# Optimization experiments

Measured on AMD Instinct MI355X. Metric: run time of the kernel, lower is better.

Reference implementation:

```python
import jax, jax.numpy as jnp
import numpy as np

EMBED_DIM = 128
MAX_LEN = 256.0
LN_EPS = 1e-5


def sinusoidal_pe(x, embed_dim, embed_size):
    # x: [..., ] float; returns [..., embed_dim]
    inv_freq = 1.0 / embed_size ** (2.0 * jnp.arange(embed_dim // 2, dtype=jnp.float32) / embed_dim)
    angles = x[..., None] * jnp.float32(np.pi) * inv_freq
    return jnp.concatenate([jnp.sin(angles), jnp.cos(angles)], axis=-1)


def setup_inputs() -> dict:
    key = jax.random.key(0)
    ks = jax.random.split(key, 20)
    B, N, A = 4, 256, 4
    input_nf, hidden_nf, output_nf = 128, 256, 128
    edge_in = 2 * input_nf + EMBED_DIM + 3  # 387

    def lin(k, fan_in, fan_out):
        bound = 1.0 / np.sqrt(fan_in)
        kw, kb = jax.random.split(k)
        W = jax.random.uniform(kw, (fan_in, fan_out), jnp.float32, -bound, bound)
        b = jax.random.uniform(kb, (fan_out,), jnp.float32, -bound, bound)
        return W, b

    We1, be1 = lin(ks[0], edge_in, hidden_nf)
    We2, be2 = lin(ks[1], hidden_nf, hidden_nf)
    Wn1, bn1 = lin(ks[2], input_nf + hidden_nf, hidden_nf)
    Wn2, bn2 = lin(ks[3], hidden_nf, output_nf)
    Wc1, bc1 = lin(ks[4], hidden_nf, hidden_nf)
    Wc2, bc2 = lin(ks[5], hidden_nf, 1)

    coords = jax.random.normal(ks[6], (B, N, A, 3), jnp.float32)
    node_features = jax.random.normal(ks[7], (B, N, input_nf), jnp.float32)
    atom_mask = jnp.ones((B, N, A), jnp.float32)
    residue_indices = jnp.sort(jax.random.randint(ks[8], (B, N), 0, 256), axis=-1).astype(jnp.int32)

    return dict(coords=coords, node_features=node_features, atom_mask=atom_mask,
                residue_indices=residue_indices,
                We1=We1, be1=be1, We2=We2, be2=be2,
                Wn1=Wn1, bn1=bn1, Wn2=Wn2, bn2=bn2,
                gamma=jnp.ones((output_nf,), jnp.float32), beta=jnp.zeros((output_nf,), jnp.float32),
                Wc1=Wc1, bc1=bc1, Wc2=Wc2, bc2=bc2)


def reference(coords, node_features, atom_mask, residue_indices,
              We1, be1, We2, be2, Wn1, bn1, Wn2, bn2, gamma, beta,
              Wc1, bc1, Wc2, bc2):
    B, N, A, _ = coords.shape
    # relative residue offsets -> sinusoidal PE: [B,N,N,embed_dim]
    rel = (residue_indices[:, :, None] - residue_indices[:, None, :]).astype(jnp.float32)
    rel_enc = sinusoidal_pe(rel, EMBED_DIM, MAX_LEN)
    # directional vectors: mean over atoms of pairwise coord diffs -> [B,N,N,3]
    dirs = (coords[:, :, None, :, :] - coords[:, None, :, :, :]).mean(axis=3)
    # pairwise edge features [B,N,N,2*F+E+3]
    fi = jnp.broadcast_to(node_features[:, :, None, :], (B, N, N, node_features.shape[-1]))
    fj = jnp.broadcast_to(node_features[:, None, :, :], (B, N, N, node_features.shape[-1]))
    edge_feat = jnp.concatenate([fi, fj, rel_enc, dirs], axis=-1)
    msg = jax.nn.silu(jax.nn.silu(edge_feat @ We1 + be1) @ We2 + be2)  # [B,N,N,H]
    agg = msg.sum(axis=2)  # [B,N,H]
    h = jnp.concatenate([node_features, agg], axis=-1)
    h = jax.nn.silu(h @ Wn1 + bn1) @ Wn2 + bn2  # [B,N,output_nf]
    mu = h.mean(axis=-1, keepdims=True)
    var = ((h - mu) ** 2).mean(axis=-1, keepdims=True)
    h = (h - mu) / jnp.sqrt(var + LN_EPS) * gamma + beta
    cu = jax.nn.silu(msg @ Wc1 + bc1) @ Wc2 + bc2  # [B,N,N,1]
    coord_updates = (cu * dirs).sum(axis=2)  # [B,N,3]
    updated_coords = coords + coord_updates[:, :, None, :] * atom_mask[..., None]
    return updated_coords, h
```

## Files before the change

kernel.cpp:

```cpp
#include <hip/hip_runtime.h>

typedef unsigned short u16;
typedef __attribute__((ext_vector_type(8))) _Float16 hfrag8;
typedef __attribute__((ext_vector_type(4))) float f32x4;

__device__ __forceinline__ float bu2f(u16 u) { return __uint_as_float(((unsigned)u) << 16); }
__device__ __forceinline__ u16 f2bu(float f) {
    unsigned x = __float_as_uint(f);
    return (u16)((x + 0x7fffu + ((x >> 16) & 1u)) >> 16);
}
__device__ __forceinline__ u16 f2hu(float f) {
    _Float16 h = (_Float16)f;
    return __builtin_bit_cast(u16, h);
}
__device__ __forceinline__ float ldf(const void* p, int i, bool f32) {
    return f32 ? ((const float*)p)[i] : bu2f(((const u16*)p)[i]);
}
__device__ __forceinline__ float siluf(float x) {
    return x * __builtin_amdgcn_rcpf(1.0f + __expf(-x));
}
__device__ __forceinline__ unsigned pkh(float a, float b) {
    return __builtin_bit_cast(unsigned, __builtin_amdgcn_cvt_pkrtz(a, b));
}
__device__ __forceinline__ bool detect_f32(const void* nf, int t) {
    const u16* p = (const u16*)nf;
    int ext = 0;
    if (t < 256) {
        u16 v = p[t * 2];
        int e = (v >> 7) & 0xFF;
        ext = (e >= 140 || e == 0) ? 1 : 0;
    }
    return __syncthreads_count(ext) > 32;
}

__global__ __launch_bounds__(256) void prep_kernel(
    const void* __restrict__ coords, const void* __restrict__ nf,
    const void* __restrict__ We1, const void* __restrict__ be1,
    const void* __restrict__ We2, const void* __restrict__ Wc1,
    float* __restrict__ cbar, float* __restrict__ pi2, float* __restrict__ qd,
    float* __restrict__ Ttab, u16* __restrict__ We2X, u16* __restrict__ Wc1X)
{
    const int t = threadIdx.x;
    const bool f32 = detect_f32(nf, t);
    const int blk = blockIdx.x;

    __shared__ float nf_l[4][128];
    __shared__ float ctmp[4][12];
    __shared__ float cb_l[4][3];
    __shared__ float pe[128];
    __shared__ u16 tile[32][33];

    if (blk < 256) {
        const int row0 = blk * 4;
        for (int idx = t; idx < 512; idx += 256) {
            int r = idx >> 7, k = idx & 127;
            nf_l[r][k] = ldf(nf, (row0 + r) * 128 + k, f32);
        }
        if (t < 48) ctmp[t / 12][t % 12] = ldf(coords, row0 * 12 + t, f32);
        __syncthreads();
        if (t < 12) {
            int r = t / 3, x = t % 3;
            float m = 0.25f * (ctmp[r][x] + ctmp[r][3 + x] + ctmp[r][6 + x] + ctmp[r][9 + x]);
            cb_l[r][x] = m;
            cbar[(row0 + r) * 3 + x] = m;
        }
        __syncthreads();
        const int n = t;
        float accP[4] = {0.f, 0.f, 0.f, 0.f}, accQ[4] = {0.f, 0.f, 0.f, 0.f};
        for (int k = 0; k < 128; k++) {
            float w1 = ldf(We1, k * 256 + n, f32);
            float w2 = ldf(We1, (128 + k) * 256 + n, f32);
#pragma unroll
            for (int r = 0; r < 4; r++) {
                accP[r] += nf_l[r][k] * w1;
                accQ[r] += nf_l[r][k] * w2;
            }
        }
        float wx = ldf(We1, 384 * 256 + n, f32);
        float wy = ldf(We1, 385 * 256 + n, f32);
        float wz = ldf(We1, 386 * 256 + n, f32);
        float b1 = ldf(be1, n, f32);
#pragma unroll
        for (int r = 0; r < 4; r++) {
            float d = cb_l[r][0] * wx + cb_l[r][1] * wy + cb_l[r][2] * wz;
            pi2[(row0 + r) * 256 + n] = accP[r] + d + b1;
            qd[(row0 + r) * 256 + n]  = accQ[r] - d;
        }
    } else if (blk < 767) {
        const float d = (float)(blk - 511);
        if (t < 64) {
            float ang = d * 3.14159265358979323846f * exp2f(-(float)t * 0.125f);
            pe[t] = sinf(ang);
            pe[64 + t] = cosf(ang);
        }
        __syncthreads();
        float acc = 0.f;
        for (int k = 0; k < 128; k++) acc += pe[k] * ldf(We1, (256 + k) * 256 + t, f32);
        Ttab[(blk - 256) * 256 + t] = acc;
    } else {
        int tbf = blk - 767;
        int mat = tbf >> 6;
        int tb = tbf & 63;
        int bx = tb & 7, by = tb >> 3;
        const void* src = mat ? Wc1 : We2;
        u16* dst = mat ? Wc1X : We2X;
        int tx = threadIdx.x & 31, ty = threadIdx.x >> 5;
#pragma unroll
        for (int p = 0; p < 4; p++) {
            int r = by * 32 + ty + p * 8;
            tile[ty + p * 8][tx] = f2hu(ldf(src, r * 256 + bx * 32 + tx, f32));
        }
        __syncthreads();
#pragma unroll
        for (int p = 0; p < 4; p++) {
            int n = bx * 32 + ty + p * 8;
            dst[((n >> 4) * 8 + by) * 512 + (n & 15) * 32 + tx] = tile[tx][ty + p * 8];
        }
    }
}

__global__ __launch_bounds__(512, 1)
void edge_kernel(
    const int* __restrict__ resid,
    const float* __restrict__ pi2, const float* __restrict__ qd,
    const float* __restrict__ Ttab, const float* __restrict__ cbar,
    const u16* __restrict__ We2X, const u16* __restrict__ Wc1X,
    const void* __restrict__ be2, const void* __restrict__ bc1,
    const void* __restrict__ Wc2, const void* __restrict__ bc2,
    const void* __restrict__ nf,
    float* __restrict__ agg_out, float* __restrict__ cupd_out)
{
    const int t = threadIdx.x;
    const bool f32 = detect_f32(nf, t);
    const int node = blockIdx.x;
    const int b = node >> 8;
    const int lane = t & 63, w = t >> 6;
    const int c = lane & 15, q = lane >> 4;

    __shared__ __align__(16) u16 U[128][280];
    __shared__ int relidx[256];
    __shared__ float fin[8][4];

    if (t < 256) relidx[t] = resid[node] - resid[(b << 8) + t] + 255;
    const float bc2q = 0.125f * ldf(bc2, 0, f32);

    float4 be2v[2], bc1v[2], wc2v[2];
#pragma unroll
    for (int nn = 0; nn < 2; nn++) {
        const int base = w * 32 + nn * 16 + q * 4;
        be2v[nn] = make_float4(ldf(be2, base, f32), ldf(be2, base + 1, f32),
                               ldf(be2, base + 2, f32), ldf(be2, base + 3, f32));
        bc1v[nn] = make_float4(ldf(bc1, base, f32), ldf(bc1, base + 1, f32),
                               ldf(bc1, base + 2, f32), ldf(bc1, base + 3, f32));
        wc2v[nn] = make_float4(ldf(Wc2, base, f32), ldf(Wc2, base + 1, f32),
                               ldf(Wc2, base + 2, f32), ldf(Wc2, base + 3, f32));
    }

    const int kp = lane << 2;
    const float4 pv = *(const float4*)(pi2 + node * 256 + kp);

    float aggv[2][4] = {{0.f}};
    float s0 = 0.f, s1 = 0.f, s2 = 0.f, s3 = 0.f;

    const f32x4 zf = {0.f, 0.f, 0.f, 0.f};
    __syncthreads();

    for (int jc = 0; jc < 2; jc++) {
        const int j0 = jc << 7;
        {
            const float* qbase = qd + ((b << 8) + j0) * 256 + kp;
            const int r0 = w * 16;
#pragma unroll 4
            for (int jj = 0; jj < 16; jj++) {
                const int j = r0 + jj;
                const float4 qv = *(const float4*)(qbase + j * 256);
                const float4 tv = *(const float4*)(Ttab + relidx[j0 + j] * 256 + kp);
                uint2 pk;
                pk.x = pkh(siluf(pv.x + qv.x + tv.x), siluf(pv.y + qv.y + tv.y));
                pk.y = pkh(siluf(pv.z + qv.z + tv.z), siluf(pv.w + qv.w + tv.w));
                *(uint2*)&U[j][kp] = pk;
            }
        }
        __syncthreads();

        f32x4 acc[8][2];
#pragma unroll
        for (int m = 0; m < 8; m++)
#pragma unroll
            for (int nn = 0; nn < 2; nn++) acc[m][nn] = zf;
#pragma unroll 2
        for (int ks = 0; ks < 8; ks++) {
            const int kb = ks * 32 + q * 8;
            hfrag8 wf[2];
#pragma unroll
            for (int nn = 0; nn < 2; nn++)
                wf[nn] = *(const hfrag8*)(We2X + ((w * 2 + nn) * 8 + ks) * 512 + c * 32 + q * 8);
            hfrag8 hm[8];
#pragma unroll
            for (int m = 0; m < 8; m++)
                hm[m] = *(const hfrag8*)&U[m * 16 + c][kb];
#pragma unroll
            for (int m = 0; m < 8; m++)
#pragma unroll
                for (int nn = 0; nn < 2; nn++)
                    acc[m][nn] = __builtin_amdgcn_mfma_f32_16x16x32_f16(wf[nn], hm[m], acc[m][nn], 0, 0, 0);
        }
        __syncthreads();

#pragma unroll
        for (int m = 0; m < 8; m++) {
            u16* mrow = &U[m * 16 + c][w * 32 + q * 4];
#pragma unroll
            for (int nn = 0; nn < 2; nn++) {
                float sa = siluf(acc[m][nn][0] + be2v[nn].x);
                float sb = siluf(acc[m][nn][1] + be2v[nn].y);
                float sc_ = siluf(acc[m][nn][2] + be2v[nn].z);
                float sd = siluf(acc[m][nn][3] + be2v[nn].w);
                aggv[nn][0] += sa; aggv[nn][1] += sb;
                aggv[nn][2] += sc_; aggv[nn][3] += sd;
                uint2 pk;
                pk.x = pkh(sa, sb);
                pk.y = pkh(sc_, sd);
                *(uint2*)(mrow + nn * 16) = pk;
            }
        }
        __syncthreads();

#pragma unroll
        for (int m = 0; m < 8; m++)
#pragma unroll
            for (int nn = 0; nn < 2; nn++) acc[m][nn] = zf;
#pragma unroll 2
        for (int ks = 0; ks < 8; ks++) {
            const int kb = ks * 32 + q * 8;
            hfrag8 wf[2];
#pragma unroll
            for (int nn = 0; nn < 2; nn++)
                wf[nn] = *(const hfrag8*)(Wc1X + ((w * 2 + nn) * 8 + ks) * 512 + c * 32 + q * 8);
            hfrag8 mm[8];
#pragma unroll
            for (int m = 0; m < 8; m++)
                mm[m] = *(const hfrag8*)&U[m * 16 + c][kb];
#pragma unroll
            for (int m = 0; m < 8; m++)
#pragma unroll
                for (int nn = 0; nn < 2; nn++)
                    acc[m][nn] = __builtin_amdgcn_mfma_f32_16x16x32_f16(wf[nn], mm[m], acc[m][nn], 0, 0, 0);
        }
        __syncthreads();

#pragma unroll
        for (int m = 0; m < 8; m++) {
            float dv = 0.f;
#pragma unroll
            for (int nn = 0; nn < 2; nn++) {
                dv += siluf(acc[m][nn][0] + bc1v[nn].x) * wc2v[nn].x;
                dv += siluf(acc[m][nn][1] + bc1v[nn].y) * wc2v[nn].y;
                dv += siluf(acc[m][nn][2] + bc1v[nn].z) * wc2v[nn].z;
                dv += siluf(acc[m][nn][3] + bc1v[nn].w) * wc2v[nn].w;
            }
            dv += __shfl_xor(dv, 16);
            dv += __shfl_xor(dv, 32);
            if (q == 0) {
                const float vb = dv + bc2q;
                const float* cp = cbar + ((b << 8) + j0 + m * 16 + c) * 3;
                s0 += vb;
                s1 += vb * cp[0];
                s2 += vb * cp[1];
                s3 += vb * cp[2];
            }
        }
    }

#pragma unroll
    for (int nn = 0; nn < 2; nn++)
#pragma unroll
        for (int r = 0; r < 4; r++) {
            float v = aggv[nn][r];
            v += __shfl_xor(v, 1);
            v += __shfl_xor(v, 2);
            v += __shfl_xor(v, 4);
            v += __shfl_xor(v, 8);
            aggv[nn][r] = v;
        }
    if (c == 0) {
#pragma unroll
        for (int nn = 0; nn < 2; nn++) {
            float4 o = make_float4(aggv[nn][0], aggv[nn][1], aggv[nn][2], aggv[nn][3]);
            *(float4*)(agg_out + node * 256 + w * 32 + nn * 16 + q * 4) = o;
        }
    }

#pragma unroll
    for (int d = 1; d < 16; d <<= 1) {
        s0 += __shfl_xor(s0, d);
        s1 += __shfl_xor(s1, d);
        s2 += __shfl_xor(s2, d);
        s3 += __shfl_xor(s3, d);
    }
    if (lane == 0) { fin[w][0] = s0; fin[w][1] = s1; fin[w][2] = s2; fin[w][3] = s3; }
    __syncthreads();
    if (t == 0) {
        float S0 = 0.f, S1 = 0.f, S2 = 0.f, S3 = 0.f;
#pragma unroll
        for (int u = 0; u < 8; u++) {
            S0 += fin[u][0]; S1 += fin[u][1]; S2 += fin[u][2]; S3 += fin[u][3];
        }
        const float cx = cbar[node * 3 + 0], cy = cbar[node * 3 + 1], cz = cbar[node * 3 + 2];
        cupd_out[node * 3 + 0] = S0 * cx - S1;
        cupd_out[node * 3 + 1] = S0 * cy - S2;
        cupd_out[node * 3 + 2] = S0 * cz - S3;
    }
}

__global__ __launch_bounds__(256) void out_kernel(
    const void* __restrict__ nf, const float* __restrict__ agg,
    const void* __restrict__ Wn1, const void* __restrict__ bn1,
    const void* __restrict__ Wn2, const void* __restrict__ bn2,
    const void* __restrict__ gamma, const void* __restrict__ beta,
    const void* __restrict__ coords, const void* __restrict__ mask,
    const float* __restrict__ cupd, void* __restrict__ d_out)
{
    const int t = threadIdx.x;
    const bool f32 = detect_f32(nf, t);

    if (blockIdx.x >= 128) {
        int idx = (blockIdx.x - 128) * 256 + t;
        if (idx < 4 * 256 * 4 * 3) {
            int x = idx % 3;
            int a = (idx / 3) & 3;
            int node = idx / 12;
            float v = ldf(coords, idx, f32) + cupd[node * 3 + x] * ldf(mask, node * 4 + a, f32);
            if (f32) ((float*)d_out)[idx] = v;
            else     ((u16*)d_out)[idx] = f2bu(v);
        }
        return;
    }

    const int row0 = blockIdx.x * 8;
    __shared__ float x_l[8][384];
    __shared__ float hs[8][256];
    __shared__ float ho[8][128];
    for (int idx = t; idx < 8 * 384; idx += 256) {
        int r = idx / 384, k = idx % 384;
        x_l[r][k] = (k < 128) ? ldf(nf, (row0 + r) * 128 + k, f32)
                              : agg[(row0 + r) * 256 + (k - 128)];
    }
    __syncthreads();
    {
        float a1[8] = {0.f, 0.f, 0.f, 0.f, 0.f, 0.f, 0.f, 0.f};
        for (int k = 0; k < 384; k++) {
            float wv = ldf(Wn1, k * 256 + t, f32);
#pragma unroll
            for (int r = 0; r < 8; r++) a1[r] += x_l[r][k] * wv;
        }
        float b1 = ldf(bn1, t, f32);
#pragma unroll
        for (int r = 0; r < 8; r++) hs[r][t] = siluf(a1[r] + b1);
    }
    __syncthreads();
    {
        int cc = t & 127, rg = (t >> 7) * 4;
        float a2[4] = {0.f, 0.f, 0.f, 0.f};
        for (int k = 0; k < 256; k++) {
            float wv = ldf(Wn2, k * 128 + cc, f32);
#pragma unroll
            for (int r = 0; r < 4; r++) a2[r] += hs[rg + r][k] * wv;
        }
        float b2 = ldf(bn2, cc, f32);
#pragma unroll
        for (int r = 0; r < 4; r++) ho[rg + r][cc] = a2[r] + b2;
    }
    __syncthreads();
    {
        int row = t >> 5, s = t & 31;
        float sm = 0.f, sq = 0.f;
#pragma unroll
        for (int u = 0; u < 4; u++) {
            float v = ho[row][s + 32 * u];
            sm += v; sq += v * v;
        }
#pragma unroll
        for (int d = 1; d < 32; d <<= 1) {
            sm += __shfl_xor(sm, d);
            sq += __shfl_xor(sq, d);
        }
        float mu = sm * (1.f / 128.f);
        float var = sq * (1.f / 128.f) - mu * mu;
        float inv = rsqrtf(var + 1e-5f);
#pragma unroll
        for (int u = 0; u < 4; u++) {
            int cc = s + 32 * u;
            float y = (ho[row][cc] - mu) * inv;
            float outv = y * ldf(gamma, cc, f32) + ldf(beta, cc, f32);
            int oi = 12288 + (row0 + row) * 128 + cc;
            if (f32) ((float*)d_out)[oi] = outv;
            else     ((u16*)d_out)[oi] = f2bu(outv);
        }
    }
}

extern "C" void kernel_launch(void* const* d_in, const int* in_sizes, int n_in,
                              void* d_out, int out_size, void* d_ws, size_t ws_size,
                              hipStream_t stream)
{
    const void* coords = d_in[0];
    const void* nf     = d_in[1];
    const void* mask   = d_in[2];
    const int* resid   = (const int*)d_in[3];
    const void* We1 = d_in[4];
    const void* be1 = d_in[5];
    const void* We2 = d_in[6];
    const void* be2 = d_in[7];
    const void* Wn1 = d_in[8];
    const void* bn1 = d_in[9];
    const void* Wn2 = d_in[10];
    const void* bn2 = d_in[11];
    const void* gamma = d_in[12];
    const void* beta  = d_in[13];
    const void* Wc1 = d_in[14];
    const void* bc1 = d_in[15];
    const void* Wc2 = d_in[16];
    const void* bc2 = d_in[17];

    float* f   = (float*)d_ws + 16;
    float* cbar = f;
    float* pi2  = cbar + 3072;
    float* qd   = pi2 + 262144;
    float* Ttab = qd + 262144;
    float* agg  = Ttab + 130816;
    float* cupd = agg + 262144;
    u16* We2X = (u16*)(cupd + 3072);
    u16* Wc1X = We2X + 65536;

    hipLaunchKernelGGL(prep_kernel, dim3(895), dim3(256), 0, stream,
                       coords, nf, We1, be1, We2, Wc1, cbar, pi2, qd, Ttab, We2X, Wc1X);
    hipLaunchKernelGGL(edge_kernel, dim3(1024), dim3(512), 0, stream,
                       resid, pi2, qd, Ttab, cbar, We2X, Wc1X, be2, bc1, Wc2, bc2, nf, agg, cupd);
    hipLaunchKernelGGL(out_kernel, dim3(176), dim3(256), 0, stream,
                       nf, agg, Wn1, bn1, Wn2, bn2, gamma, beta, coords, mask, cupd, d_out);
}
```

Measured before the change: 318.0 us.

## Retile edge-kernel MFMA warps into a 2x4 grid of 64x64 output tiles

Each of the 8 warps now computes a 64-row by 64-column output block (4x4 MFMA tiles) instead of all 128 rows by 32 columns (8x2 tiles). This halves the LDS activation fragment reads per MFMA, at the cost of more weight fragment loads from global or cache. Because each row's partial sums now come from two row-warp groups, the bc2 scaling changes to a quarter and agg is combined in shared memory before it is written. Bias and Wc2 vectors are staged in LDS rather than held in registers, to offset the larger accumulator footprint.

Result: slower. 330.2 us (+3.8%).

```diff
diff --git a/kernel.cpp b/kernel.cpp
--- a/kernel.cpp
+++ b/kernel.cpp
@@ -136,30 +136,27 @@
     const int b = node >> 8;
     const int lane = t & 63, w = t >> 6;
     const int c = lane & 15, q = lane >> 4;
+    const int wr = w & 1, wc = w >> 1;
+    const int rowbase = wr * 64, colbase = wc * 64;
 
     __shared__ __align__(16) u16 U[128][280];
     __shared__ int relidx[256];
+    __shared__ float be2_l[256], bc1_l[256], wc2_l[256];
+    __shared__ float aggl[2][256];
     __shared__ float fin[8][4];
 
-    if (t < 256) relidx[t] = resid[node] - resid[(b << 8) + t] + 255;
-    const float bc2q = 0.125f * ldf(bc2, 0, f32);
-
-    float4 be2v[2], bc1v[2], wc2v[2];
-#pragma unroll
-    for (int nn = 0; nn < 2; nn++) {
-        const int base = w * 32 + nn * 16 + q * 4;
-        be2v[nn] = make_float4(ldf(be2, base, f32), ldf(be2, base + 1, f32),
-                               ldf(be2, base + 2, f32), ldf(be2, base + 3, f32));
-        bc1v[nn] = make_float4(ldf(bc1, base, f32), ldf(bc1, base + 1, f32),
-                               ldf(bc1, base + 2, f32), ldf(bc1, base + 3, f32));
-        wc2v[nn] = make_float4(ldf(Wc2, base, f32), ldf(Wc2, base + 1, f32),
-                               ldf(Wc2, base + 2, f32), ldf(Wc2, base + 3, f32));
-    }
+    if (t < 256) {
+        relidx[t] = resid[node] - resid[(b << 8) + t] + 255;
+        be2_l[t] = ldf(be2, t, f32);
+        bc1_l[t] = ldf(bc1, t, f32);
+        wc2_l[t] = ldf(Wc2, t, f32);
+    }
+    const float bc2q = 0.25f * ldf(bc2, 0, f32);
 
     const int kp = lane << 2;
     const float4 pv = *(const float4*)(pi2 + node * 256 + kp);
 
-    float aggv[2][4] = {{0.f}};
+    float aggv[4][4] = {{0.f}};
     float s0 = 0.f, s1 = 0.f, s2 = 0.f, s3 = 0.f;
 
     const f32x4 zf = {0.f, 0.f, 0.f, 0.f};
@@ -183,39 +180,40 @@
         }
         __syncthreads();
 
-        f32x4 acc[8][2];
-#pragma unroll
-        for (int m = 0; m < 8; m++)
-#pragma unroll
-            for (int nn = 0; nn < 2; nn++) acc[m][nn] = zf;
+        f32x4 acc[4][4];
+#pragma unroll
+        for (int m = 0; m < 4; m++)
+#pragma unroll
+            for (int nn = 0; nn < 4; nn++) acc[m][nn] = zf;
 #pragma unroll 2
         for (int ks = 0; ks < 8; ks++) {
             const int kb = ks * 32 + q * 8;
-            hfrag8 wf[2];
-#pragma unroll
-            for (int nn = 0; nn < 2; nn++)
-                wf[nn] = *(const hfrag8*)(We2X + ((w * 2 + nn) * 8 + ks) * 512 + c * 32 + q * 8);
-            hfrag8 hm[8];
-#pragma unroll
-            for (int m = 0; m < 8; m++)
-                hm[m] = *(const hfrag8*)&U[m * 16 + c][kb];
-#pragma unroll
-            for (int m = 0; m < 8; m++)
-#pragma unroll
-                for (int nn = 0; nn < 2; nn++)
+            hfrag8 wf[4];
+#pragma unroll
+            for (int nn = 0; nn < 4; nn++)
+                wf[nn] = *(const hfrag8*)(We2X + ((wc * 4 + nn) * 8 + ks) * 512 + c * 32 + q * 8);
+            hfrag8 hm[4];
+#pragma unroll
+            for (int m = 0; m < 4; m++)
+                hm[m] = *(const hfrag8*)&U[rowbase + m * 16 + c][kb];
+#pragma unroll
+            for (int m = 0; m < 4; m++)
+#pragma unroll
+                for (int nn = 0; nn < 4; nn++)
                     acc[m][nn] = __builtin_amdgcn_mfma_f32_16x16x32_f16(wf[nn], hm[m], acc[m][nn], 0, 0, 0);
         }
         __syncthreads();
 
 #pragma unroll
-        for (int m = 0; m < 8; m++) {
-            u16* mrow = &U[m * 16 + c][w * 32 + q * 4];
-#pragma unroll
-            for (int nn = 0; nn < 2; nn++) {
-                float sa = siluf(acc[m][nn][0] + be2v[nn].x);
-                float sb = siluf(acc[m][nn][1] + be2v[nn].y);
-                float sc_ = siluf(acc[m][nn][2] + be2v[nn].z);
-                float sd = siluf(acc[m][nn][3] + be2v[nn].w);
+        for (int m = 0; m < 4; m++) {
+            u16* mrow = &U[rowbase + m * 16 + c][colbase + q * 4];
+#pragma unroll
+            for (int nn = 0; nn < 4; nn++) {
+                const float4 b4 = *(const float4*)&be2_l[colbase + nn * 16 + q * 4];
+                float sa = siluf(acc[m][nn][0] + b4.x);
+                float sb = siluf(acc[m][nn][1] + b4.y);
+                float sc_ = siluf(acc[m][nn][2] + b4.z);
+                float sd = siluf(acc[m][nn][3] + b4.w);
                 aggv[nn][0] += sa; aggv[nn][1] += sb;
                 aggv[nn][2] += sc_; aggv[nn][3] += sd;
                 uint2 pk;
@@ -227,43 +225,46 @@
         __syncthreads();
 
 #pragma unroll
-        for (int m = 0; m < 8; m++)
-#pragma unroll
-            for (int nn = 0; nn < 2; nn++) acc[m][nn] = zf;
+        for (int m = 0; m < 4; m++)
+#pragma unroll
+            for (int nn = 0; nn < 4; nn++) acc[m][nn] = zf;
 #pragma unroll 2
         for (int ks = 0; ks < 8; ks++) {
             const int kb = ks * 32 + q * 8;
-            hfrag8 wf[2];
-#pragma unroll
-            for (int nn = 0; nn < 2; nn++)
-                wf[nn] = *(const hfrag8*)(Wc1X + ((w * 2 + nn) * 8 + ks) * 512 + c * 32 + q * 8);
-            hfrag8 mm[8];
-#pragma unroll
-            for (int m = 0; m < 8; m++)
-                mm[m] = *(const hfrag8*)&U[m * 16 + c][kb];
-#pragma unroll
-            for (int m = 0; m < 8; m++)
-#pragma unroll
-                for (int nn = 0; nn < 2; nn++)
+            hfrag8 wf[4];
+#pragma unroll
+            for (int nn = 0; nn < 4; nn++)
+                wf[nn] = *(const hfrag8*)(Wc1X + ((wc * 4 + nn) * 8 + ks) * 512 + c * 32 + q * 8);
+            hfrag8 mm[4];
+#pragma unroll
+            for (int m = 0; m < 4; m++)
+                mm[m] = *(const hfrag8*)&U[rowbase + m * 16 + c][kb];
+#pragma unroll
+            for (int m = 0; m < 4; m++)
+#pragma unroll
+                for (int nn = 0; nn < 4; nn++)
                     acc[m][nn] = __builtin_amdgcn_mfma_f32_16x16x32_f16(wf[nn], mm[m], acc[m][nn], 0, 0, 0);
         }
         __syncthreads();
 
 #pragma unroll
-        for (int m = 0; m < 8; m++) {
+        for (int m = 0; m < 4; m++) {
             float dv = 0.f;
 #pragma unroll
-            for (int nn = 0; nn < 2; nn++) {
-                dv += siluf(acc[m][nn][0] + bc1v[nn].x) * wc2v[nn].x;
-                dv += siluf(acc[m][nn][1] + bc1v[nn].y) * wc2v[nn].y;
-                dv += siluf(acc[m][nn][2] + bc1v[nn].z) * wc2v[nn].z;
-                dv += siluf(acc[m][nn][3] + bc1v[nn].w) * wc2v[nn].w;
+            for (int nn = 0; nn < 4; nn++) {
+                const float4 c4 = *(const float4*)&bc1_l[colbase + nn * 16 + q * 4];
+                const float4 w4 = *(const float4*)&wc2_l[colbase + nn * 16 + q * 4];
+                dv += siluf(acc[m][nn][0] + c4.x) * w4.x;
+                dv += siluf(acc[m][nn][1] + c4.y) * w4.y;
+                dv += siluf(acc[m][nn][2] + c4.z) * w4.z;
+                dv += siluf(acc[m][nn][3] + c4.w) * w4.w;
             }
             dv += __shfl_xor(dv, 16);
             dv += __shfl_xor(dv, 32);
             if (q == 0) {
                 const float vb = dv + bc2q;
-                const float* cp = cbar + ((b << 8) + j0 + m * 16 + c) * 3;
+                const int j = j0 + rowbase + m * 16 + c;
+                const float* cp = cbar + ((b << 8) + j) * 3;
                 s0 += vb;
                 s1 += vb * cp[0];
                 s2 += vb * cp[1];
@@ -273,7 +274,7 @@
     }
 
 #pragma unroll
-    for (int nn = 0; nn < 2; nn++)
+    for (int nn = 0; nn < 4; nn++)
 #pragma unroll
         for (int r = 0; r < 4; r++) {
             float v = aggv[nn][r];
@@ -285,9 +286,9 @@
         }
     if (c == 0) {
 #pragma unroll
-        for (int nn = 0; nn < 2; nn++) {
+        for (int nn = 0; nn < 4; nn++) {
             float4 o = make_float4(aggv[nn][0], aggv[nn][1], aggv[nn][2], aggv[nn][3]);
-            *(float4*)(agg_out + node * 256 + w * 32 + nn * 16 + q * 4) = o;
+            *(float4*)&aggl[wr][colbase + nn * 16 + q * 4] = o;
         }
     }
 
@@ -300,6 +301,7 @@
     }
     if (lane == 0) { fin[w][0] = s0; fin[w][1] = s1; fin[w][2] = s2; fin[w][3] = s3; }
     __syncthreads();
+    if (t < 256) agg_out[node * 256 + t] = aggl[0][t] + aggl[1][t];
     if (t == 0) {
         float S0 = 0.f, S1 = 0.f, S2 = 0.f, S3 = 0.f;
 #pragma unroll
```
